# Kernel optimization log

Hardware: AMD Instinct MI355X
Metric: run time of the kernel (lower is better)

Reference implementation:

```python
import jax, jax.numpy as jnp
import numpy as np

B, S, D = 4, 2048, 1024
H = 16
HD = D // H

def setup_inputs() -> dict:
    key = jax.random.key(0)
    ks = jax.random.split(key, 6)
    scale = 0.02
    return {
        "x": jax.random.normal(ks[0], (B, S, D), dtype=jnp.float32),
        "W_q": jax.random.normal(ks[1], (D, D), dtype=jnp.float32) * scale,
        "W_k": jax.random.normal(ks[2], (D, D), dtype=jnp.float32) * scale,
        "W_v": jax.random.normal(ks[3], (D, D), dtype=jnp.float32) * scale,
        "W_o": jax.random.normal(ks[4], (D, D), dtype=jnp.float32) * scale,
        "b_o": jax.random.normal(ks[5], (D,), dtype=jnp.float32) * scale,
    }

def reference(x, W_q, W_k, W_v, W_o, b_o):
    b, s, d = x.shape
    # projections, split heads: [b, h, s, hd]
    q = (x @ W_q).reshape(b, s, H, HD).transpose(0, 2, 1, 3)
    k = (x @ W_k).reshape(b, s, H, HD).transpose(0, 2, 1, 3)
    v = (x @ W_v).reshape(b, s, H, HD).transpose(0, 2, 1, 3)
    scores = jnp.einsum('bhqd,bhkd->bhqk', q, k)
    causal = jnp.triu(jnp.ones((s, s), dtype=bool), k=1)
    scores = jnp.where(causal, -jnp.inf, scores)
    # module divides by sqrt(hd) after masking; -inf stays -inf
    attn = jax.nn.softmax(scores / jnp.sqrt(jnp.float32(HD)), axis=-1)
    ctx = jnp.einsum('bhqk,bhkd->bhqd', attn, v)
    ctx = ctx.transpose(0, 2, 1, 3).reshape(b, s, d)
    return ctx @ W_o + b_o
```

## Files before the change

### kernel.cpp

```cpp
#include <hip/hip_runtime.h>
#include <hip/hip_bf16.h>
#include <math.h>

typedef __attribute__((ext_vector_type(8))) short bf16x8;
typedef __attribute__((ext_vector_type(4))) float f32x4;
typedef unsigned short u16;
typedef __hip_bfloat16 HB;

#define B_ 4
#define S_ 2048
#define D_ 1024
#define H_ 16
#define HD_ 64

__device__ __forceinline__ u16 f2b(float f) {
  HB h = __float2bfloat16(f);
  return *reinterpret_cast<u16*>(&h);
}
__device__ __forceinline__ void store1(HB* p, float v) { *p = __float2bfloat16(v); }
__device__ __forceinline__ void store1(float* p, float v) { *p = v; }

__device__ __forceinline__ float fexp2(float x) {
#if __has_builtin(__builtin_amdgcn_exp2f)
  return __builtin_amdgcn_exp2f(x);
#else
  return exp2f(x);
#endif
}

__device__ __forceinline__ void glds16(const u16* g, u16* l) {
  __builtin_amdgcn_global_load_lds(
      (const __attribute__((address_space(1))) void*)g,
      (__attribute__((address_space(3))) void*)l, 16, 0, 0);
}

__global__ __launch_bounds__(256) void cast_x(const float* __restrict__ xin,
                                              u16* __restrict__ xout) {
  const long i0 = ((long)blockIdx.x * 256 + threadIdx.x) * 8;
  bf16x8 r;
#pragma unroll
  for (int j = 0; j < 8; ++j) r[j] = (short)f2b(xin[i0 + j]);
  *(bf16x8*)(xout + i0) = r;
}

__global__ __launch_bounds__(256) void transpose_w(
    const float* __restrict__ w0, const float* __restrict__ w1,
    const float* __restrict__ w2, const float* __restrict__ w3,
    u16* __restrict__ out) {
  __shared__ __align__(16) u16 T[64 * 72];
  const float* Ws[4] = {w0, w1, w2, w3};
  const float* W = Ws[blockIdx.z];
  u16* Wt = out + (long)blockIdx.z * (1 << 20);
  const int t = threadIdx.x;
  const int r = t >> 3;
  const int c8 = (t & 7) * 8;
#pragma unroll
  for (int it = 0; it < 2; ++it) {
    const int row = blockIdx.y * 64 + it * 32 + r;
    const float* src = W + (long)row * D_ + blockIdx.x * 64 + c8;
#pragma unroll
    for (int j = 0; j < 8; ++j) T[(c8 + j) * 72 + it * 32 + r] = f2b(src[j]);
  }
  __syncthreads();
#pragma unroll
  for (int it = 0; it < 2; ++it) {
    const int row = it * 32 + r;
    bf16x8 v = *(const bf16x8*)(&T[row * 72 + c8]);
    *(bf16x8*)(Wt + (long)(blockIdx.x * 64 + row) * D_ + blockIdx.y * 64 + c8) = v;
  }
}

template <typename OT>
__global__ __launch_bounds__(256) void gemm_bt128d(
    const u16* __restrict__ A, const u16* __restrict__ BTb, long bt_stride,
    OT* __restrict__ Cb, long c_stride, const float* __restrict__ bias,
    u16* __restrict__ vt, int scale_q, int M, int N, int K) {
  const int flat = ((int)blockIdx.z << 9) + ((int)blockIdx.y << 3) + blockIdx.x;
  const int cpx = ((int)gridDim.z << 9) >> 3;
  const int nf = (flat & 7) * cpx + (flat >> 3);
  const int bz = nf >> 9;
  const int rem = nf & 511;
  const int by = rem >> 3, bx = rem & 7;

  const u16* BT = BTb + (long)bz * bt_stride;
  OT* C = Cb + (long)bz * c_stride;

  __shared__ __align__(16) u16 As[2][128 * 64];
  __shared__ __align__(16) u16 Bs[2][128 * 64];

  const int tid = threadIdx.x;
  const int w = tid >> 6, lane = tid & 63;
  const int qr = lane & 15, quad = lane >> 4;
  const int wm = w >> 1, wn = w & 1;

  const long rowA0 = (long)by * 128;
  const long rowB0 = (long)bx * 128;

  const int sr8 = lane >> 3;
  const int sc8 = ((lane & 7) ^ sr8) * 8;

  f32x4 acc[4][4] = {};

#define STAGE(nb, k0)                                                      \
  {                                                                        \
    _Pragma("unroll") for (int t = 0; t < 4; ++t) {                        \
      const int r = w * 32 + t * 8;                                        \
      glds16(A + (rowA0 + r + sr8) * K + (k0) + sc8, &As[nb][r * 64]);     \
      glds16(BT + (rowB0 + r + sr8) * K + (k0) + sc8, &Bs[nb][r * 64]);    \
    }                                                                      \
  }

  STAGE(0, 0);
  __syncthreads();

  const int NT = K >> 6;
  for (int kt = 0; kt < NT; ++kt) {
    const int b = kt & 1;
    if (kt + 1 < NT) STAGE(b ^ 1, (kt + 1) << 6);

#pragma unroll
    for (int kk = 0; kk < 2; ++kk) {
      bf16x8 af[4], bf[4];
#pragma unroll
      for (int ms = 0; ms < 4; ++ms) {
        const int m = wm * 64 + ms * 16 + qr;
        af[ms] = *(const bf16x8*)(&As[b][m * 64 +
                                         (((kk * 4 + quad) ^ (m & 7)) * 8)]);
      }
#pragma unroll
      for (int ns = 0; ns < 4; ++ns) {
        const int n = wn * 64 + ns * 16 + qr;
        bf[ns] = *(const bf16x8*)(&Bs[b][n * 64 +
                                         (((kk * 4 + quad) ^ (n & 7)) * 8)]);
      }
#pragma unroll
      for (int ms = 0; ms < 4; ++ms)
#pragma unroll
        for (int ns = 0; ns < 4; ++ns)
          acc[ms][ns] = __builtin_amdgcn_mfma_f32_16x16x32_bf16(
              af[ms], bf[ns], acc[ms][ns], 0, 0, 0);
    }
    __syncthreads();
  }
#undef STAGE

  if (vt && bz == 2) {
#pragma unroll
    for (int ns = 0; ns < 4; ++ns) {
      const int col = (int)rowB0 + wn * 64 + ns * 16 + qr;
#pragma unroll
      for (int ms = 0; ms < 4; ++ms) {
        const long row = rowA0 + wm * 64 + ms * 16 + quad * 4;
        const long b = row >> 11, s = row & 2047;
        ushort4 pk;
        pk.x = f2b(acc[ms][ns][0]); pk.y = f2b(acc[ms][ns][1]);
        pk.z = f2b(acc[ms][ns][2]); pk.w = f2b(acc[ms][ns][3]);
        *(ushort4*)(vt + ((b * H_ + (col >> 6)) * HD_ + (col & 63)) * S_ + s) = pk;
      }
    }
    return;
  }

  const float qs = (scale_q && bz == 0) ? 0.18033688011112042f : 1.f;
#pragma unroll
  for (int ns = 0; ns < 4; ++ns) {
    const long col = rowB0 + wn * 64 + ns * 16 + qr;
    const float bv = bias ? bias[col] : 0.f;
#pragma unroll
    for (int ms = 0; ms < 4; ++ms) {
      const long row = rowA0 + wm * 64 + ms * 16 + quad * 4;
#pragma unroll
      for (int r = 0; r < 4; ++r)
        store1(&C[(row + r) * (long)N + col], acc[ms][ns][r] * qs + bv);
    }
  }
}

__global__ __launch_bounds__(256) void attn7(
    const u16* __restrict__ Q, const u16* __restrict__ Kg,
    const u16* __restrict__ Vt, u16* __restrict__ ctx) {
  __shared__ __align__(16) u16 KV[2][2][64 * 64];
  __shared__ __align__(16) u16 Pl[4][16 * 64];

  const int tid = threadIdx.x;
  const int w = tid >> 6, lane = tid & 63;
  const int qr = lane & 15, quad = lane >> 4;
  const int bh = blockIdx.x;
  const int b = bh >> 4, h = bh & 15;

  const long baseQK = ((long)b * S_) * D_ + h * HD_;
  const long baseVt = (long)bh * HD_ * S_;

  const int sr8 = lane >> 3;
  const int sc8 = ((lane & 7) ^ sr8) * 8;

  const int qp = 15 - (int)blockIdx.y;
  const int q0 = qp * 128;
  const int qbase = q0 + w * 32;

  bf16x8 aq[2][2];
#pragma unroll
  for (int i = 0; i < 2; ++i) {
    const u16* qp_ = Q + baseQK + (long)(qbase + i * 16 + qr) * D_;
    aq[i][0] = *(const bf16x8*)(qp_ + quad * 8);
    aq[i][1] = *(const bf16x8*)(qp_ + 32 + quad * 8);
  }

  float li[2] = {};
  f32x4 o[2][4] = {};

  const int nkt = q0 / 64 + 2;

#pragma unroll
  for (int t = 0; t < 2; ++t) {
    const int r = t * 32 + w * 8 + sr8;
    glds16(Kg + baseQK + (long)r * D_ + sc8, &KV[0][0][(t * 32 + w * 8) * 64]);
    glds16(Vt + baseVt + (long)r * S_ + sc8, &KV[0][1][(t * 32 + w * 8) * 64]);
  }

  for (int kt = 0; kt < nkt; ++kt) {
    const int kbase = kt * 64;
    const int buf = kt & 1;

    __syncthreads();

    if (kt + 1 < nkt) {
      const int nb = kbase + 64;
#pragma unroll
      for (int t = 0; t < 2; ++t) {
        const int r = t * 32 + w * 8 + sr8;
        glds16(Kg + baseQK + (long)(nb + r) * D_ + sc8,
               &KV[buf ^ 1][0][(t * 32 + w * 8) * 64]);
        glds16(Vt + baseVt + (long)r * S_ + nb + sc8,
               &KV[buf ^ 1][1][(t * 32 + w * 8) * 64]);
      }
    }

    const u16* Ksb = KV[buf][0];
    const u16* Vsb = KV[buf][1];

    bf16x8 kf[4][2];
#pragma unroll
    for (int ns = 0; ns < 4; ++ns) {
      const int row = ns * 16 + qr;
      kf[ns][0] = *(const bf16x8*)(&Ksb[row * 64 + ((quad ^ (row & 7)) * 8)]);
      kf[ns][1] =
          *(const bf16x8*)(&Ksb[row * 64 + (((4 + quad) ^ (row & 7)) * 8)]);
    }

    f32x4 s[2][4] = {};
#pragma unroll
    for (int i = 0; i < 2; ++i)
#pragma unroll
      for (int ns = 0; ns < 4; ++ns) {
        s[i][ns] = __builtin_amdgcn_mfma_f32_16x16x32_bf16(
            kf[ns][0], aq[i][0], s[i][ns], 0, 0, 0);
        s[i][ns] = __builtin_amdgcn_mfma_f32_16x16x32_bf16(
            kf[ns][1], aq[i][1], s[i][ns], 0, 0, 0);
      }

#pragma unroll
    for (int i = 0; i < 2; ++i) {
      if (kbase + 64 > qbase + i * 16) {
        const int qrow = qbase + i * 16 + qr;
#pragma unroll
        for (int ns = 0; ns < 4; ++ns) {
          const int kc = kbase + ns * 16 + quad * 4;
#pragma unroll
          for (int r = 0; r < 4; ++r)
            if (kc + r > qrow) s[i][ns][r] = -1.0e30f;
        }
      }
    }

    bf16x8 vf[4][2];
#pragma unroll
    for (int ns = 0; ns < 4; ++ns) {
      const int row = ns * 16 + qr;
      vf[ns][0] = *(const bf16x8*)(&Vsb[row * 64 + ((quad ^ (row & 7)) * 8)]);
      vf[ns][1] =
          *(const bf16x8*)(&Vsb[row * 64 + (((4 + quad) ^ (row & 7)) * 8)]);
    }

#pragma unroll
    for (int i = 0; i < 2; ++i) {
      float ps = 0.f;
#pragma unroll
      for (int ns = 0; ns < 4; ++ns) {
        const float p0 = fexp2(s[i][ns][0]);
        const float p1 = fexp2(s[i][ns][1]);
        const float p2 = fexp2(s[i][ns][2]);
        const float p3 = fexp2(s[i][ns][3]);
        ps += (p0 + p1) + (p2 + p3);
        ushort4 pk;
        pk.x = f2b(p0); pk.y = f2b(p1); pk.z = f2b(p2); pk.w = f2b(p3);
        *(ushort4*)(&Pl[w][qr * 64 +
                           (((2 * ns + (quad >> 1)) ^ (qr & 7)) * 8) +
                           (quad & 1) * 4]) = pk;
      }
      ps += __shfl_xor(ps, 16, 64);
      ps += __shfl_xor(ps, 32, 64);
      li[i] += ps;

      bf16x8 pf0 = *(const bf16x8*)(&Pl[w][qr * 64 + ((quad ^ (qr & 7)) * 8)]);
      bf16x8 pf1 =
          *(const bf16x8*)(&Pl[w][qr * 64 + (((4 + quad) ^ (qr & 7)) * 8)]);
#pragma unroll
      for (int ns = 0; ns < 4; ++ns) {
        o[i][ns] = __builtin_amdgcn_mfma_f32_16x16x32_bf16(pf0, vf[ns][0],
                                                           o[i][ns], 0, 0, 0);
        o[i][ns] = __builtin_amdgcn_mfma_f32_16x16x32_bf16(pf1, vf[ns][1],
                                                           o[i][ns], 0, 0, 0);
      }
    }
  }

#pragma unroll
  for (int i = 0; i < 2; ++i)
#pragma unroll
    for (int r = 0; r < 4; ++r) {
      const float inv = 1.f / __shfl(li[i], quad * 4 + r, 64);
      const long row = qbase + i * 16 + quad * 4 + r;
#pragma unroll
      for (int ns = 0; ns < 4; ++ns)
        ctx[((long)b * S_ + row) * D_ + h * HD_ + ns * 16 + qr] =
            f2b(o[i][ns][r] * inv);
    }
}

extern "C" void kernel_launch(void* const* d_in, const int* in_sizes, int n_in,
                              void* d_out, int out_size, void* d_ws,
                              size_t ws_size, hipStream_t stream) {
  const float* x  = (const float*)d_in[0];
  const float* Wq = (const float*)d_in[1];
  const float* Wk = (const float*)d_in[2];
  const float* Wv = (const float*)d_in[3];
  const float* Wo = (const float*)d_in[4];
  const float* bo = (const float*)d_in[5];

  u16* ws = (u16*)d_ws;
  u16* xb  = ws;
  u16* Wt  = xb + 8388608l;
  u16* Qb  = Wt + 4l * 1048576;
  u16* Kb  = Qb + 8388608l;
  u16* Vb  = Kb + 8388608l;
  u16* ctx = Qb;

  cast_x<<<4096, 256, 0, stream>>>(x, xb);

  transpose_w<<<dim3(16, 16, 4), 256, 0, stream>>>(Wq, Wk, Wv, Wo, Wt);

  gemm_bt128d<HB><<<dim3(8, 64, 3), 256, 0, stream>>>(
      xb, Wt, 1048576l, (HB*)Qb, 8388608l, nullptr, Vb, 1, 8192, 1024, 1024);

  attn7<<<dim3(64, 16), 256, 0, stream>>>(Qb, Kb, Vb, ctx);

  gemm_bt128d<float><<<dim3(8, 64, 1), 256, 0, stream>>>(
      ctx, Wt + 3l * 1048576, 0, (float*)d_out, 0, bo, nullptr, 0,
      8192, 1024, 1024);
}
```

Measured before the change: 252.6 us.

## Load K/V fragments directly from global and compute row sums via MFMA

```diff
diff --git a/kernel.cpp b/kernel.cpp
--- a/kernel.cpp
+++ b/kernel.cpp
@@ -176,10 +176,9 @@
   }
 }
 
-__global__ __launch_bounds__(256) void attn7(
+__global__ __launch_bounds__(256) void attn9(
     const u16* __restrict__ Q, const u16* __restrict__ Kg,
     const u16* __restrict__ Vt, u16* __restrict__ ctx) {
-  __shared__ __align__(16) u16 KV[2][2][64 * 64];
   __shared__ __align__(16) u16 Pl[4][16 * 64];
 
   const int tid = threadIdx.x;
@@ -191,9 +190,6 @@
   const long baseQK = ((long)b * S_) * D_ + h * HD_;
   const long baseVt = (long)bh * HD_ * S_;
 
-  const int sr8 = lane >> 3;
-  const int sc8 = ((lane & 7) ^ sr8) * 8;
-
   const int qp = 15 - (int)blockIdx.y;
   const int q0 = qp * 128;
   const int qbase = q0 + w * 32;
@@ -206,46 +202,26 @@
     aq[i][1] = *(const bf16x8*)(qp_ + 32 + quad * 8);
   }
 
-  float li[2] = {};
+  bf16x8 vones;
+#pragma unroll
+  for (int j = 0; j < 8; ++j) vones[j] = (short)0x3F80;
+
+  f32x4 li[2] = {};
   f32x4 o[2][4] = {};
 
   const int nkt = q0 / 64 + 2;
-
-#pragma unroll
-  for (int t = 0; t < 2; ++t) {
-    const int r = t * 32 + w * 8 + sr8;
-    glds16(Kg + baseQK + (long)r * D_ + sc8, &KV[0][0][(t * 32 + w * 8) * 64]);
-    glds16(Vt + baseVt + (long)r * S_ + sc8, &KV[0][1][(t * 32 + w * 8) * 64]);
-  }
 
   for (int kt = 0; kt < nkt; ++kt) {
     const int kbase = kt * 64;
-    const int buf = kt & 1;
-
-    __syncthreads();
-
-    if (kt + 1 < nkt) {
-      const int nb = kbase + 64;
-#pragma unroll
-      for (int t = 0; t < 2; ++t) {
-        const int r = t * 32 + w * 8 + sr8;
-        glds16(Kg + baseQK + (long)(nb + r) * D_ + sc8,
-               &KV[buf ^ 1][0][(t * 32 + w * 8) * 64]);
-        glds16(Vt + baseVt + (long)r * S_ + nb + sc8,
-               &KV[buf ^ 1][1][(t * 32 + w * 8) * 64]);
-      }
-    }
-
-    const u16* Ksb = KV[buf][0];
-    const u16* Vsb = KV[buf][1];
+    const u16* Kt = Kg + baseQK + (long)kbase * D_;
+    const u16* Vp = Vt + baseVt + kbase;
 
     bf16x8 kf[4][2];
 #pragma unroll
     for (int ns = 0; ns < 4; ++ns) {
-      const int row = ns * 16 + qr;
-      kf[ns][0] = *(const bf16x8*)(&Ksb[row * 64 + ((quad ^ (row & 7)) * 8)]);
-      kf[ns][1] =
-          *(const bf16x8*)(&Ksb[row * 64 + (((4 + quad) ^ (row & 7)) * 8)]);
+      const u16* kr = Kt + (long)(ns * 16 + qr) * D_ + quad * 8;
+      kf[ns][0] = *(const bf16x8*)(kr);
+      kf[ns][1] = *(const bf16x8*)(kr + 32);
     }
 
     f32x4 s[2][4] = {};
@@ -259,6 +235,14 @@
             kf[ns][1], aq[i][1], s[i][ns], 0, 0, 0);
       }
 
+    bf16x8 vf[4][2];
+#pragma unroll
+    for (int ns = 0; ns < 4; ++ns) {
+      const u16* vr = Vp + (long)(ns * 16 + qr) * S_ + quad * 8;
+      vf[ns][0] = *(const bf16x8*)(vr);
+      vf[ns][1] = *(const bf16x8*)(vr + 32);
+    }
+
 #pragma unroll
     for (int i = 0; i < 2; ++i) {
       if (kbase + 64 > qbase + i * 16) {
@@ -273,34 +257,19 @@
       }
     }
 
-    bf16x8 vf[4][2];
-#pragma unroll
-    for (int ns = 0; ns < 4; ++ns) {
-      const int row = ns * 16 + qr;
-      vf[ns][0] = *(const bf16x8*)(&Vsb[row * 64 + ((quad ^ (row & 7)) * 8)]);
-      vf[ns][1] =
-          *(const bf16x8*)(&Vsb[row * 64 + (((4 + quad) ^ (row & 7)) * 8)]);
-    }
-
 #pragma unroll
     for (int i = 0; i < 2; ++i) {
-      float ps = 0.f;
 #pragma unroll
       for (int ns = 0; ns < 4; ++ns) {
-        const float p0 = fexp2(s[i][ns][0]);
-        const float p1 = fexp2(s[i][ns][1]);
-        const float p2 = fexp2(s[i][ns][2]);
-        const float p3 = fexp2(s[i][ns][3]);
-        ps += (p0 + p1) + (p2 + p3);
         ushort4 pk;
-        pk.x = f2b(p0); pk.y = f2b(p1); pk.z = f2b(p2); pk.w = f2b(p3);
+        pk.x = f2b(fexp2(s[i][ns][0]));
+        pk.y = f2b(fexp2(s[i][ns][1]));
+        pk.z = f2b(fexp2(s[i][ns][2]));
+        pk.w = f2b(fexp2(s[i][ns][3]));
         *(ushort4*)(&Pl[w][qr * 64 +
                            (((2 * ns + (quad >> 1)) ^ (qr & 7)) * 8) +
                            (quad & 1) * 4]) = pk;
       }
-      ps += __shfl_xor(ps, 16, 64);
-      ps += __shfl_xor(ps, 32, 64);
-      li[i] += ps;
 
       bf16x8 pf0 = *(const bf16x8*)(&Pl[w][qr * 64 + ((quad ^ (qr & 7)) * 8)]);
       bf16x8 pf1 =
@@ -312,6 +281,8 @@
         o[i][ns] = __builtin_amdgcn_mfma_f32_16x16x32_bf16(pf1, vf[ns][1],
                                                            o[i][ns], 0, 0, 0);
       }
+      li[i] = __builtin_amdgcn_mfma_f32_16x16x32_bf16(pf0, vones, li[i], 0, 0, 0);
+      li[i] = __builtin_amdgcn_mfma_f32_16x16x32_bf16(pf1, vones, li[i], 0, 0, 0);
     }
   }
 
@@ -319,7 +290,7 @@
   for (int i = 0; i < 2; ++i)
 #pragma unroll
     for (int r = 0; r < 4; ++r) {
-      const float inv = 1.f / __shfl(li[i], quad * 4 + r, 64);
+      const float inv = 1.f / li[i][r];
       const long row = qbase + i * 16 + quad * 4 + r;
 #pragma unroll
       for (int ns = 0; ns < 4; ++ns)
@@ -353,7 +324,7 @@
   gemm_bt128d<HB><<<dim3(8, 64, 3), 256, 0, stream>>>(
       xb, Wt, 1048576l, (HB*)Qb, 8388608l, nullptr, Vb, 1, 8192, 1024, 1024);
 
-  attn7<<<dim3(64, 16), 256, 0, stream>>>(Qb, Kb, Vb, ctx);
+  attn9<<<dim3(64, 16), 256, 0, stream>>>(Qb, Kb, Vb, ctx);
 
   gemm_bt128d<float><<<dim3(8, 64, 1), 256, 0, stream>>>(
       ctx, Wt + 3l * 1048576, 0, (float*)d_out, 0, bo, nullptr, 0,
```

New measurement: 318.3 us. 26.0% more time.
